# Performance work log

Measured on AMD Instinct MI355X. Metric: run time of the kernel, lower is better.

The kernel has to match this reference:

```python
import jax, jax.numpy as jnp
import numpy as np

D_MODEL = 1024
NUM_HEADS = 16
DEPTH = D_MODEL // NUM_HEADS


def setup_inputs() -> dict:
    key = jax.random.key(0)
    ks = jax.random.split(key, 11)
    B, S = 4, 2048
    scale = 1.0 / np.sqrt(D_MODEL)
    inp = {
        "query": jax.random.normal(ks[0], (B, S, D_MODEL), jnp.float32),
        "key": jax.random.normal(ks[1], (B, S, D_MODEL), jnp.float32),
        "value": jax.random.normal(ks[2], (B, S, D_MODEL), jnp.float32),
        # Linear params (torch nn.Linear: y = x @ W.T + b); store W as [out, in]
        "wq_w": jax.random.normal(ks[3], (D_MODEL, D_MODEL), jnp.float32) * scale,
        "wq_b": jnp.zeros((D_MODEL,), jnp.float32),
        "wk_w": jax.random.normal(ks[4], (D_MODEL, D_MODEL), jnp.float32) * scale,
        "wk_b": jnp.zeros((D_MODEL,), jnp.float32),
        "wv_w": jax.random.normal(ks[5], (D_MODEL, D_MODEL), jnp.float32) * scale,
        "wv_b": jnp.zeros((D_MODEL,), jnp.float32),
        "dense_w": jax.random.normal(ks[6], (D_MODEL, D_MODEL), jnp.float32) * scale,
        "dense_b": jnp.zeros((D_MODEL,), jnp.float32),
    }
    return inp


def _split_heads(x, B):
    # [B, S, D] -> [B, H, S, depth]
    return x.reshape(B, -1, NUM_HEADS, DEPTH).transpose(0, 2, 1, 3)


def reference(query, key, value, wq_w, wq_b, wk_w, wk_b, wv_w, wv_b, dense_w, dense_b):
    B = query.shape[0]
    q = _split_heads(query @ wq_w.T + wq_b, B)   # [B,H,Sq,depth]
    k = _split_heads(key @ wk_w.T + wk_b, B)     # [B,H,Sk,depth]
    v = _split_heads(value @ wv_w.T + wv_b, B)   # [B,H,Sk,depth]
    scores = jnp.einsum("bhqd,bhkd->bhqk", q, k) / jnp.sqrt(jnp.float32(DEPTH)).astype(q.dtype)
    attn = jax.nn.softmax(scores, axis=-1)
    out = jnp.einsum("bhqk,bhkd->bhqd", attn, v)  # [B,H,Sq,depth]
    out = out.transpose(0, 2, 1, 3).reshape(B, -1, D_MODEL)
    return out @ dense_w.T + dense_b
```

## Files before the change

kernel.cpp:

```cpp
#include <hip/hip_runtime.h>
#include <hip/hip_bf16.h>
#include <stdint.h>


#define SEQ    2048
#define DEPTH  64
#define HEADS  16
#define NMODEL 1024
#define MROWS  8192

typedef __bf16 bf16x8 __attribute__((ext_vector_type(8)));
typedef float  f32x4  __attribute__((ext_vector_type(4)));

__device__ __forceinline__ unsigned short f32_bf16(float f) {
    union { float f; unsigned int u; } c; c.f = f;
    unsigned int u = c.u + 0x7FFFu + ((c.u >> 16) & 1u);
    return (unsigned short)(u >> 16);
}

__device__ __forceinline__ void gload16(const unsigned short* g, unsigned short* l) {
    __builtin_amdgcn_global_load_lds(
        (const __attribute__((address_space(1))) unsigned int*)g,
        (__attribute__((address_space(3))) unsigned int*)l, 16, 0, 0);
}

__global__ __launch_bounds__(256) void cvt_flat_kernel(
    const float* __restrict__ a0, const float* __restrict__ a1, const float* __restrict__ a2,
    const float* __restrict__ w0, const float* __restrict__ w1,
    const float* __restrict__ w2, const float* __restrict__ w3,
    unsigned short* __restrict__ oa0, unsigned short* __restrict__ oa1,
    unsigned short* __restrict__ oa2,
    unsigned short* __restrict__ ow0, unsigned short* __restrict__ ow1,
    unsigned short* __restrict__ ow2, unsigned short* __restrict__ ow3)
{
    const unsigned int i = blockIdx.x * 256u + threadIdx.x;
    const unsigned int NA = 1u << 21;
    const unsigned int AW = 3u * NA;
    const float* in; unsigned short* out; unsigned int idx;
    if (i < AW) {
        const unsigned int p = i >> 21; idx = i & (NA - 1u);
        in  = (p == 0) ? a0 : (p == 1) ? a1 : a2;
        out = (p == 0) ? oa0 : (p == 1) ? oa1 : oa2;
    } else {
        const unsigned int j = i - AW;
        const unsigned int p = j >> 18; idx = j & ((1u << 18) - 1u);
        in  = (p == 0) ? w0 : (p == 1) ? w1 : (p == 2) ? w2 : w3;
        out = (p == 0) ? ow0 : (p == 1) ? ow1 : (p == 2) ? ow2 : ow3;
    }
    float4 f = ((const float4*)in)[idx];
    ushort4 o;
    o.x = f32_bf16(f.x); o.y = f32_bf16(f.y);
    o.z = f32_bf16(f.z); o.w = f32_bf16(f.w);
    ((ushort4*)out)[idx] = o;
}

__device__ __forceinline__ void gemm256_core(
    const unsigned short* __restrict__ A, const unsigned short* __restrict__ W,
    const float* __restrict__ bias, void* __restrict__ outp,
    int mode, float scale, int m0, int n0,
    unsigned short* __restrict__ Alds, unsigned short* __restrict__ Blds)
{
    const int tid  = threadIdx.x;
    const int wave = tid >> 6, lane = tid & 63;
    const int l15  = lane & 15, quad = lane >> 4;
    const int wr   = wave >> 1, wc = wave & 1;
    const int swz  = l15 & 7;
    const int K    = 1024;

    f32x4 acc[4][4] = {};

    const int trow = tid >> 3;
    const int tg   = ((tid & 7) ^ (trow & 7)) << 3;
    const unsigned short* Asrc[2][2];
    const unsigned short* Bsrc[2];
    #pragma unroll
    for (int u = 0; u < 2; ++u) {
        #pragma unroll
        for (int s = 0; s < 2; ++s)
            Asrc[u][s] = A + (size_t)(m0 + u * 128 + s * 64 + trow) * K + tg;
        Bsrc[u] = W + (size_t)(n0 + u * 64 + trow) * K + tg;
    }

    auto STAGE = [&](int buf, int kt2) {
        unsigned short* Ad = Alds + buf * 16384;
        unsigned short* Bd = Blds + buf * 8192;
        gload16(Asrc[0][0] + kt2 * 64, Ad + (      wave * 8) * 64);
        gload16(Asrc[0][1] + kt2 * 64, Ad + ( 64 + wave * 8) * 64);
        gload16(Asrc[1][0] + kt2 * 64, Ad + (128 + wave * 8) * 64);
        gload16(Asrc[1][1] + kt2 * 64, Ad + (192 + wave * 8) * 64);
        gload16(Bsrc[0]    + kt2 * 64, Bd + (      wave * 8) * 64);
        gload16(Bsrc[1]    + kt2 * 64, Bd + ( 64 + wave * 8) * 64);
    };

    STAGE(0, 0);
    STAGE(1, 1);
    asm volatile("s_waitcnt vmcnt(6)" ::: "memory");
    __builtin_amdgcn_s_barrier();

    const int arow = wr * 64 + l15;
    const int brow = wc * 64 + l15;

    for (int kt = 0; kt < 16; ++kt) {
        const unsigned short* Ab = Alds + (kt % 3) * 16384;
        const unsigned short* Bb = Blds + (kt % 3) * 8192;

        bf16x8 a0[4], b0[4];
        {
            const int pg = ((quad ^ swz) << 3);
            #pragma unroll
            for (int j = 0; j < 4; ++j)
                b0[j] = *(const bf16x8*)&Bb[(brow + j * 16) * 64 + pg];
            #pragma unroll
            for (int i = 0; i < 4; ++i)
                a0[i] = *(const bf16x8*)&Ab[(arow + i * 16) * 64 + pg];
        }
        if (kt + 2 < 16) STAGE((kt + 2) % 3, kt + 2);

        __builtin_amdgcn_s_setprio(1);
        #pragma unroll
        for (int i = 0; i < 4; ++i)
            #pragma unroll
            for (int j = 0; j < 4; ++j)
                acc[i][j] = __builtin_amdgcn_mfma_f32_16x16x32_bf16(a0[i], b0[j], acc[i][j], 0, 0, 0);
        __builtin_amdgcn_s_setprio(0);

        bf16x8 a1[4], b1[4];
        {
            const int pg = (((4 + quad) ^ swz) << 3);
            #pragma unroll
            for (int j = 0; j < 4; ++j)
                b1[j] = *(const bf16x8*)&Bb[(brow + j * 16) * 64 + pg];
            #pragma unroll
            for (int i = 0; i < 4; ++i)
                a1[i] = *(const bf16x8*)&Ab[(arow + i * 16) * 64 + pg];
        }
        __builtin_amdgcn_s_setprio(1);
        #pragma unroll
        for (int i = 0; i < 4; ++i)
            #pragma unroll
            for (int j = 0; j < 4; ++j)
                acc[i][j] = __builtin_amdgcn_mfma_f32_16x16x32_bf16(a1[i], b1[j], acc[i][j], 0, 0, 0);
        __builtin_amdgcn_s_setprio(0);

        if (kt + 2 < 16)
            asm volatile("s_waitcnt vmcnt(6)" ::: "memory");
        else
            asm volatile("s_waitcnt vmcnt(0)" ::: "memory");
        __builtin_amdgcn_s_barrier();
    }

    #pragma unroll
    for (int i = 0; i < 4; ++i) {
        #pragma unroll
        for (int j = 0; j < 4; ++j) {
            const int col = n0 + wc * 64 + j * 16 + l15;
            const int row_b = m0 + wr * 64 + i * 16 + quad * 4;
            if (mode == 2) {
                const int colp = (col & ~31)
                               | (col & 3)
                               | (((col >> 4) & 1) << 2)
                               | (((col >> 2) & 3) << 3);
                #pragma unroll
                for (int r = 0; r < 4; ++r) {
                    const int row = row_b + r;
                    ((unsigned short*)outp)[(size_t)row * MROWS + colp] =
                        f32_bf16(acc[i][j][r] + bias[row]);
                }
            } else if (mode == 0) {
                const float bv = bias[col];
                #pragma unroll
                for (int r = 0; r < 4; ++r)
                    ((float*)outp)[(size_t)(row_b + r) * NMODEL + col] = acc[i][j][r] + bv;
            } else {
                const float bv = bias[col];
                const int h_ = col >> 6, d_ = col & 63;
                #pragma unroll
                for (int r = 0; r < 4; ++r) {
                    const int row = row_b + r;
                    const int b_ = row >> 11, s_ = row & 2047;
                    ((unsigned short*)outp)[(((size_t)(b_ * HEADS + h_) * SEQ + s_) << 6) + d_] =
                        f32_bf16((acc[i][j][r] + bv) * scale);
                }
            }
        }
    }
}

__global__ __launch_bounds__(512, 2) void gemm_qkv(
    const unsigned short* __restrict__ qb,  const unsigned short* __restrict__ wqb,
    const float* __restrict__ bq, unsigned short* __restrict__ Qp,
    const unsigned short* __restrict__ kb,  const unsigned short* __restrict__ wkb,
    const float* __restrict__ bk, unsigned short* __restrict__ Kpj,
    const unsigned short* __restrict__ wvb, const unsigned short* __restrict__ vb,
    const float* __restrict__ bv, unsigned short* __restrict__ Vtg,
    float qscale)
{
    __shared__ unsigned short Alds[3 * 256 * 64];
    __shared__ unsigned short Blds[3 * 128 * 64];
    const int o = blockIdx.x, z = blockIdx.y;
    const int sid = (o & 7) * 32 + (o >> 3);
    if (z == 0) {
        gemm256_core(qb, wqb, bq, Qp, 1, qscale, (sid >> 3) * 256, (sid & 7) * 128, Alds, Blds);
    } else if (z == 1) {
        gemm256_core(kb, wkb, bk, Kpj, 1, 1.0f, (sid >> 3) * 256, (sid & 7) * 128, Alds, Blds);
    } else {
        gemm256_core(wvb, vb, bv, Vtg, 2, 1.0f, (sid & 3) * 256, (sid >> 2) * 128, Alds, Blds);
    }
}

__global__ __launch_bounds__(512, 2) void gemm_dense(
    const unsigned short* __restrict__ A, const unsigned short* __restrict__ W,
    const float* __restrict__ bias, float* __restrict__ out)
{
    __shared__ unsigned short Alds[3 * 256 * 64];
    __shared__ unsigned short Blds[3 * 128 * 64];
    const int o = blockIdx.x;
    const int sid = (o & 7) * 32 + (o >> 3);
    gemm256_core(A, W, bias, out, 0, 1.0f, (sid >> 3) * 256, (sid & 7) * 128, Alds, Blds);
}

__global__ __launch_bounds__(256, 2) void attn_fwd(
    const unsigned short* __restrict__ Qp,
    const unsigned short* __restrict__ Kp,
    const unsigned short* __restrict__ Vtg,
    unsigned short* __restrict__ Op)
{
    __shared__ unsigned short Klds[3 * 64 * 64];
    __shared__ unsigned short Vlds[3 * 64 * 64];
    const int tid  = threadIdx.x;
    const int wave = tid >> 6, lane = tid & 63;
    const int l15  = lane & 15, quad = lane >> 4;
    const int swz  = l15 & 7;
    const int bh   = blockIdx.y;
    const int b_   = bh >> 4, h_ = bh & 15;
    const int q0   = blockIdx.x * 256;

    const unsigned short* Qb = Qp + (size_t)bh * SEQ * DEPTH;
    const unsigned short* Kb = Kp + (size_t)bh * SEQ * DEPTH;
    const unsigned short* Vb = Vtg + (size_t)h_ * DEPTH * MROWS + (size_t)b_ * SEQ;

    const int srow = (wave << 3) + (lane >> 3);
    const int scg  = (lane & 7) ^ ((lane >> 3) & 7);

    const unsigned short* Kg0 = Kb + (size_t)srow * DEPTH + scg * 8;
    const unsigned short* Kg1 = Kb + (size_t)(srow + 32) * DEPTH + scg * 8;
    const unsigned short* Vg0 = Vb + (size_t)srow * MROWS + scg * 8;
    const unsigned short* Vg1 = Vb + (size_t)(srow + 32) * MROWS + scg * 8;

    bf16x8 qf[4][2];
    #pragma unroll
    for (int i = 0; i < 4; ++i)
        #pragma unroll
        for (int kc = 0; kc < 2; ++kc)
            qf[i][kc] = *(const bf16x8*)(Qb + (size_t)(q0 + wave * 64 + i * 16 + l15) * DEPTH
                                         + kc * 32 + quad * 8);

    union { bf16x8 v; unsigned short s[8]; } uo;
    #pragma unroll
    for (int j = 0; j < 8; ++j) uo.s[j] = 0x3F80;
    const bf16x8 ones = uo.v;

    f32x4 Ot[4][4] = {};
    f32x4 lacc[4]  = {};

    auto STAGE = [&](int buf, int kt) {
        unsigned short* KW = &Klds[buf * 4096 + wave * 512];
        unsigned short* VW = &Vlds[buf * 4096 + wave * 512];
        gload16(Kg0 + (size_t)kt * 4096, KW);
        gload16(Kg1 + (size_t)kt * 4096, KW + 2048);
        gload16(Vg0 + kt * 64, VW);
        gload16(Vg1 + kt * 64, VW + 2048);
    };

    STAGE(0, 0);
    STAGE(1, 1);
    asm volatile("s_waitcnt vmcnt(4)" ::: "memory");
    __builtin_amdgcn_s_barrier();

    const int NT = SEQ / 64;
    for (int kt = 0; kt < NT; ++kt) {
        const unsigned short* Kc = &Klds[(kt % 3) * 4096];
        const unsigned short* Vc = &Vlds[(kt % 3) * 4096];
        if (kt + 2 < NT) STAGE((kt + 2) % 3, kt + 2);

        f32x4 S[2][2][4];
        __builtin_amdgcn_s_setprio(1);
        #pragma unroll
        for (int half = 0; half < 2; ++half) {
            const int r0 = (2 * half) * 16 + l15;
            const int r1 = (2 * half + 1) * 16 + l15;
            bf16x8 ka0 = *(const bf16x8*)&Kc[r0 * 64 + ((quad ^ swz) << 3)];
            bf16x8 ka1 = *(const bf16x8*)&Kc[r0 * 64 + (((4 + quad) ^ swz) << 3)];
            bf16x8 kb0 = *(const bf16x8*)&Kc[r1 * 64 + ((quad ^ swz) << 3)];
            bf16x8 kb1 = *(const bf16x8*)&Kc[r1 * 64 + (((4 + quad) ^ swz) << 3)];
            #pragma unroll
            for (int i = 0; i < 4; ++i) {
                S[half][0][i] = f32x4{};
                S[half][0][i] = __builtin_amdgcn_mfma_f32_16x16x32_bf16(ka0, qf[i][0], S[half][0][i], 0, 0, 0);
                S[half][0][i] = __builtin_amdgcn_mfma_f32_16x16x32_bf16(ka1, qf[i][1], S[half][0][i], 0, 0, 0);
                S[half][1][i] = f32x4{};
                S[half][1][i] = __builtin_amdgcn_mfma_f32_16x16x32_bf16(kb0, qf[i][0], S[half][1][i], 0, 0, 0);
                S[half][1][i] = __builtin_amdgcn_mfma_f32_16x16x32_bf16(kb1, qf[i][1], S[half][1][i], 0, 0, 0);
            }
        }
        __builtin_amdgcn_s_setprio(0);

        bf16x8 pf0[4];
        #pragma unroll
        for (int i = 0; i < 4; ++i) {
            float e0 = __builtin_amdgcn_exp2f(S[0][0][i][0]);
            float e1 = __builtin_amdgcn_exp2f(S[0][0][i][1]);
            float e2 = __builtin_amdgcn_exp2f(S[0][0][i][2]);
            float e3 = __builtin_amdgcn_exp2f(S[0][0][i][3]);
            float e4 = __builtin_amdgcn_exp2f(S[0][1][i][0]);
            float e5 = __builtin_amdgcn_exp2f(S[0][1][i][1]);
            float e6 = __builtin_amdgcn_exp2f(S[0][1][i][2]);
            float e7 = __builtin_amdgcn_exp2f(S[0][1][i][3]);
            union { bf16x8 v; __hip_bfloat162 h[4]; } up;
            up.h[0] = __float22bfloat162_rn(make_float2(e0, e1));
            up.h[1] = __float22bfloat162_rn(make_float2(e2, e3));
            up.h[2] = __float22bfloat162_rn(make_float2(e4, e5));
            up.h[3] = __float22bfloat162_rn(make_float2(e6, e7));
            pf0[i] = up.v;
        }

        __builtin_amdgcn_s_setprio(1);
        lacc[0] = __builtin_amdgcn_mfma_f32_16x16x32_bf16(ones, pf0[0], lacc[0], 0, 0, 0);
        lacc[1] = __builtin_amdgcn_mfma_f32_16x16x32_bf16(ones, pf0[1], lacc[1], 0, 0, 0);
        lacc[2] = __builtin_amdgcn_mfma_f32_16x16x32_bf16(ones, pf0[2], lacc[2], 0, 0, 0);
        lacc[3] = __builtin_amdgcn_mfma_f32_16x16x32_bf16(ones, pf0[3], lacc[3], 0, 0, 0);
        #pragma unroll
        for (int dd = 0; dd < 4; ++dd) {
            bf16x8 vf = *(const bf16x8*)&Vc[(dd * 16 + l15) * 64 + ((quad ^ swz) << 3)];
            #pragma unroll
            for (int i = 0; i < 4; ++i)
                Ot[i][dd] = __builtin_amdgcn_mfma_f32_16x16x32_bf16(vf, pf0[i], Ot[i][dd], 0, 0, 0);
        }
        __builtin_amdgcn_s_setprio(0);

        bf16x8 pf1[4];
        #pragma unroll
        for (int i = 0; i < 4; ++i) {
            float e0 = __builtin_amdgcn_exp2f(S[1][0][i][0]);
            float e1 = __builtin_amdgcn_exp2f(S[1][0][i][1]);
            float e2 = __builtin_amdgcn_exp2f(S[1][0][i][2]);
            float e3 = __builtin_amdgcn_exp2f(S[1][0][i][3]);
            float e4 = __builtin_amdgcn_exp2f(S[1][1][i][0]);
            float e5 = __builtin_amdgcn_exp2f(S[1][1][i][1]);
            float e6 = __builtin_amdgcn_exp2f(S[1][1][i][2]);
            float e7 = __builtin_amdgcn_exp2f(S[1][1][i][3]);
            union { bf16x8 v; __hip_bfloat162 h[4]; } up;
            up.h[0] = __float22bfloat162_rn(make_float2(e0, e1));
            up.h[1] = __float22bfloat162_rn(make_float2(e2, e3));
            up.h[2] = __float22bfloat162_rn(make_float2(e4, e5));
            up.h[3] = __float22bfloat162_rn(make_float2(e6, e7));
            pf1[i] = up.v;
        }

        __builtin_amdgcn_s_setprio(1);
        lacc[0] = __builtin_amdgcn_mfma_f32_16x16x32_bf16(ones, pf1[0], lacc[0], 0, 0, 0);
        lacc[1] = __builtin_amdgcn_mfma_f32_16x16x32_bf16(ones, pf1[1], lacc[1], 0, 0, 0);
        lacc[2] = __builtin_amdgcn_mfma_f32_16x16x32_bf16(ones, pf1[2], lacc[2], 0, 0, 0);
        lacc[3] = __builtin_amdgcn_mfma_f32_16x16x32_bf16(ones, pf1[3], lacc[3], 0, 0, 0);
        #pragma unroll
        for (int dd = 0; dd < 4; ++dd) {
            bf16x8 vf = *(const bf16x8*)&Vc[(dd * 16 + l15) * 64 + (((4 + quad) ^ swz) << 3)];
            #pragma unroll
            for (int i = 0; i < 4; ++i)
                Ot[i][dd] = __builtin_amdgcn_mfma_f32_16x16x32_bf16(vf, pf1[i], Ot[i][dd], 0, 0, 0);
        }
        __builtin_amdgcn_s_setprio(0);

        if (kt + 2 < NT)
            asm volatile("s_waitcnt vmcnt(4)" ::: "memory");
        else
            asm volatile("s_waitcnt vmcnt(0)" ::: "memory");
        __builtin_amdgcn_s_barrier();
    }

    #pragma unroll
    for (int i = 0; i < 4; ++i) {
        const float inv = 1.0f / lacc[i][0];
        const int row = b_ * SEQ + q0 + wave * 64 + i * 16 + l15;
        #pragma unroll
        for (int dd = 0; dd < 4; ++dd) {
            ushort4 ov;
            ov.x = f32_bf16(Ot[i][dd][0] * inv);
            ov.y = f32_bf16(Ot[i][dd][1] * inv);
            ov.z = f32_bf16(Ot[i][dd][2] * inv);
            ov.w = f32_bf16(Ot[i][dd][3] * inv);
            const int col = h_ * 64 + dd * 16 + quad * 4;
            *(ushort4*)&Op[(size_t)row * NMODEL + col] = ov;
        }
    }
}

extern "C" void kernel_launch(void* const* d_in, const int* in_sizes, int n_in,
                              void* d_out, int out_size, void* d_ws, size_t ws_size,
                              hipStream_t stream) {
    const float* q  = (const float*)d_in[0];
    const float* k  = (const float*)d_in[1];
    const float* v  = (const float*)d_in[2];
    const float* wq = (const float*)d_in[3];
    const float* bq = (const float*)d_in[4];
    const float* wk = (const float*)d_in[5];
    const float* bk = (const float*)d_in[6];
    const float* wv = (const float*)d_in[7];
    const float* bv = (const float*)d_in[8];
    const float* wd = (const float*)d_in[9];
    const float* bd = (const float*)d_in[10];

    char* ws = (char*)d_ws;
    size_t off = 0;
    auto alloc = [&](size_t bytes) { char* p = ws + off; off += bytes; return p; };
    const size_t ACT = (size_t)MROWS * NMODEL * 2;
    const size_t WGT = (size_t)NMODEL * NMODEL * 2;

    unsigned short* qb   = (unsigned short*)alloc(ACT);
    unsigned short* kb   = (unsigned short*)alloc(ACT);
    unsigned short* vb   = (unsigned short*)alloc(ACT);
    unsigned short* wqb  = (unsigned short*)alloc(WGT);
    unsigned short* wkb  = (unsigned short*)alloc(WGT);
    unsigned short* wvb  = (unsigned short*)alloc(WGT);
    unsigned short* wdb  = (unsigned short*)alloc(WGT);
    unsigned short* Qp   = (unsigned short*)alloc(ACT);
    unsigned short* Kpj  = (unsigned short*)alloc(ACT);
    unsigned short* Vtg  = (unsigned short*)alloc(ACT);
    unsigned short* attn = (unsigned short*)alloc(ACT);

    cvt_flat_kernel<<<28672, 256, 0, stream>>>(
        q, k, v, wq, wk, wv, wd, qb, kb, vb, wqb, wkb, wvb, wdb);

    const float SC = 0.18033688011112042f;
    gemm_qkv<<<dim3(256, 3), 512, 0, stream>>>(qb, wqb, bq, Qp,
                                               kb, wkb, bk, Kpj,
                                               wvb, vb, bv, Vtg, SC);

    attn_fwd<<<dim3(SEQ / 256, 64), 256, 0, stream>>>(Qp, Kpj, Vtg, attn);

    gemm_dense<<<256, 512, 0, stream>>>(attn, wdb, bd, (float*)d_out);
}
```

Baseline: 319.0 us.

## Enlarge GEMM tiles to 256x256 with eight-phase ping-pong LDS pipeline

```diff
diff --git a/kernel.cpp b/kernel.cpp
--- a/kernel.cpp
+++ b/kernel.cpp
@@ -11,6 +11,8 @@
 
 typedef __bf16 bf16x8 __attribute__((ext_vector_type(8)));
 typedef float  f32x4  __attribute__((ext_vector_type(4)));
+
+#define MFMA16 __builtin_amdgcn_mfma_f32_16x16x32_bf16
 
 __device__ __forceinline__ unsigned short f32_bf16(float f) {
     union { float f; unsigned int u; } c; c.f = f;
@@ -58,103 +60,93 @@
     const unsigned short* __restrict__ A, const unsigned short* __restrict__ W,
     const float* __restrict__ bias, void* __restrict__ outp,
     int mode, float scale, int m0, int n0,
-    unsigned short* __restrict__ Alds, unsigned short* __restrict__ Blds)
+    unsigned short* __restrict__ Abuf, unsigned short* __restrict__ Bbuf)
 {
     const int tid  = threadIdx.x;
     const int wave = tid >> 6, lane = tid & 63;
     const int l15  = lane & 15, quad = lane >> 4;
-    const int wr   = wave >> 1, wc = wave & 1;
+    const int wr   = wave >> 2, wc = wave & 3;
     const int swz  = l15 & 7;
     const int K    = 1024;
 
-    f32x4 acc[4][4] = {};
+    f32x4 acc[8][4] = {};
 
     const int trow = tid >> 3;
     const int tg   = ((tid & 7) ^ (trow & 7)) << 3;
-    const unsigned short* Asrc[2][2];
-    const unsigned short* Bsrc[2];
+    const int dstw = wave * 512;
+
+    const unsigned short* Asw[4];
+    const unsigned short* Bsw[4];
     #pragma unroll
-    for (int u = 0; u < 2; ++u) {
-        #pragma unroll
-        for (int s = 0; s < 2; ++s)
-            Asrc[u][s] = A + (size_t)(m0 + u * 128 + s * 64 + trow) * K + tg;
-        Bsrc[u] = W + (size_t)(n0 + u * 64 + trow) * K + tg;
-    }
-
-    auto STAGE = [&](int buf, int kt2) {
-        unsigned short* Ad = Alds + buf * 16384;
-        unsigned short* Bd = Blds + buf * 8192;
-        gload16(Asrc[0][0] + kt2 * 64, Ad + (      wave * 8) * 64);
-        gload16(Asrc[0][1] + kt2 * 64, Ad + ( 64 + wave * 8) * 64);
-        gload16(Asrc[1][0] + kt2 * 64, Ad + (128 + wave * 8) * 64);
-        gload16(Asrc[1][1] + kt2 * 64, Ad + (192 + wave * 8) * 64);
-        gload16(Bsrc[0]    + kt2 * 64, Bd + (      wave * 8) * 64);
-        gload16(Bsrc[1]    + kt2 * 64, Bd + ( 64 + wave * 8) * 64);
-    };
-
-    STAGE(0, 0);
-    STAGE(1, 1);
-    asm volatile("s_waitcnt vmcnt(6)" ::: "memory");
+    for (int sw = 0; sw < 4; ++sw) {
+        Asw[sw] = A + (size_t)(m0 + sw * 64 + trow) * K + tg;
+        const int rp  = sw * 64 + trow;
+        const int nh  = rp >> 7, wcb = (rp >> 5) & 3, rem = rp & 31;
+        Bsw[sw] = W + (size_t)(n0 + wcb * 64 + nh * 32 + rem) * K + tg;
+    }
+
+#define SA_(c, sw, kt) gload16(Asw[sw] + (kt) * 64, Abuf + (c) * 16384 + (sw) * 4096 + dstw)
+#define SB_(c, sw, kt) gload16(Bsw[sw] + (kt) * 64, Bbuf + (c) * 16384 + (sw) * 4096 + dstw)
+
+    SA_(0, 0, 0); SA_(0, 1, 0); SA_(0, 2, 0); SA_(0, 3, 0);
+    SB_(0, 0, 0); SB_(0, 1, 0); SB_(0, 2, 0); SB_(0, 3, 0);
+    SB_(1, 0, 1); SB_(1, 1, 1); SA_(1, 0, 1); SA_(1, 2, 1);
+    asm volatile("s_waitcnt vmcnt(4)" ::: "memory");
     __builtin_amdgcn_s_barrier();
 
-    const int arow = wr * 64 + l15;
-    const int brow = wc * 64 + l15;
-
-    for (int kt = 0; kt < 16; ++kt) {
-        const unsigned short* Ab = Alds + (kt % 3) * 16384;
-        const unsigned short* Bb = Blds + (kt % 3) * 8192;
-
-        bf16x8 a0[4], b0[4];
-        {
-            const int pg = ((quad ^ swz) << 3);
-            #pragma unroll
-            for (int j = 0; j < 4; ++j)
-                b0[j] = *(const bf16x8*)&Bb[(brow + j * 16) * 64 + pg];
-            #pragma unroll
-            for (int i = 0; i < 4; ++i)
-                a0[i] = *(const bf16x8*)&Ab[(arow + i * 16) * 64 + pg];
-        }
-        if (kt + 2 < 16) STAGE((kt + 2) % 3, kt + 2);
-
-        __builtin_amdgcn_s_setprio(1);
-        #pragma unroll
-        for (int i = 0; i < 4; ++i)
-            #pragma unroll
-            for (int j = 0; j < 4; ++j)
-                acc[i][j] = __builtin_amdgcn_mfma_f32_16x16x32_bf16(a0[i], b0[j], acc[i][j], 0, 0, 0);
-        __builtin_amdgcn_s_setprio(0);
-
-        bf16x8 a1[4], b1[4];
-        {
-            const int pg = (((4 + quad) ^ swz) << 3);
-            #pragma unroll
-            for (int j = 0; j < 4; ++j)
-                b1[j] = *(const bf16x8*)&Bb[(brow + j * 16) * 64 + pg];
-            #pragma unroll
-            for (int i = 0; i < 4; ++i)
-                a1[i] = *(const bf16x8*)&Ab[(arow + i * 16) * 64 + pg];
-        }
-        __builtin_amdgcn_s_setprio(1);
-        #pragma unroll
-        for (int i = 0; i < 4; ++i)
-            #pragma unroll
-            for (int j = 0; j < 4; ++j)
-                acc[i][j] = __builtin_amdgcn_mfma_f32_16x16x32_bf16(a1[i], b1[j], acc[i][j], 0, 0, 0);
-        __builtin_amdgcn_s_setprio(0);
-
-        if (kt + 2 < 16)
-            asm volatile("s_waitcnt vmcnt(6)" ::: "memory");
-        else
-            asm volatile("s_waitcnt vmcnt(0)" ::: "memory");
-        __builtin_amdgcn_s_barrier();
-    }
+#define PHASE_(c, mh, nh, STG, DOVM) do {                                        \
+    const unsigned short* Ab_ = Abuf + (c) * 16384;                              \
+    const unsigned short* Bb_ = Bbuf + (c) * 16384;                              \
+    bf16x8 a_[4][2], b_[2][2];                                                   \
+    _Pragma("unroll")                                                            \
+    for (int i4 = 0; i4 < 4; ++i4) {                                             \
+        const int row = wr * 128 + ((mh) * 4 + i4) * 16 + l15;                   \
+        a_[i4][0] = *(const bf16x8*)&Ab_[row * 64 + ((quad ^ swz) << 3)];        \
+        a_[i4][1] = *(const bf16x8*)&Ab_[row * 64 + (((4 + quad) ^ swz) << 3)];  \
+    }                                                                            \
+    _Pragma("unroll")                                                            \
+    for (int j2 = 0; j2 < 2; ++j2) {                                             \
+        const int row = (nh) * 128 + wc * 32 + j2 * 16 + l15;                    \
+        b_[j2][0] = *(const bf16x8*)&Bb_[row * 64 + ((quad ^ swz) << 3)];        \
+        b_[j2][1] = *(const bf16x8*)&Bb_[row * 64 + (((4 + quad) ^ swz) << 3)];  \
+    }                                                                            \
+    STG;                                                                         \
+    __builtin_amdgcn_s_barrier();                                                \
+    __builtin_amdgcn_s_setprio(1);                                               \
+    _Pragma("unroll")                                                            \
+    for (int i4 = 0; i4 < 4; ++i4)                                               \
+        _Pragma("unroll")                                                        \
+        for (int j2 = 0; j2 < 2; ++j2) {                                         \
+            acc[(mh)*4+i4][(nh)*2+j2] = MFMA16(a_[i4][0], b_[j2][0], acc[(mh)*4+i4][(nh)*2+j2], 0, 0, 0); \
+            acc[(mh)*4+i4][(nh)*2+j2] = MFMA16(a_[i4][1], b_[j2][1], acc[(mh)*4+i4][(nh)*2+j2], 0, 0, 0); \
+        }                                                                        \
+    __builtin_amdgcn_s_setprio(0);                                               \
+    if (DOVM) asm volatile("s_waitcnt vmcnt(4)" ::: "memory");                   \
+    __builtin_amdgcn_s_barrier();                                                \
+} while (0)
+
+    for (int it = 0; it < 8; ++it) {
+        const int t1 = 2 * it + 1, t2 = 2 * it + 2, t3 = 2 * it + 3;
+        const bool h2 = t2 < 16, h3 = t3 < 16;
+        PHASE_(0, 0, 0, { SA_(1, 1, t1); SA_(1, 3, t1); }, false);
+        PHASE_(0, 1, 0, { SB_(1, 2, t1); SB_(1, 3, t1); }, false);
+        PHASE_(0, 0, 1, { if (h2) { SB_(0, 0, t2); SB_(0, 1, t2); } }, false);
+        PHASE_(0, 1, 1, { if (h2) { SA_(0, 0, t2); SA_(0, 2, t2); } }, true);
+        PHASE_(1, 0, 0, { if (h2) { SA_(0, 1, t2); SA_(0, 3, t2); } }, false);
+        PHASE_(1, 1, 0, { if (h2) { SB_(0, 2, t2); SB_(0, 3, t2); } }, false);
+        PHASE_(1, 0, 1, { if (h3) { SB_(1, 0, t3); SB_(1, 1, t3); } }, false);
+        PHASE_(1, 1, 1, { if (h3) { SA_(1, 0, t3); SA_(1, 2, t3); } }, it + 1 < 8);
+    }
+#undef PHASE_
+#undef SA_
+#undef SB_
 
     #pragma unroll
-    for (int i = 0; i < 4; ++i) {
+    for (int i = 0; i < 8; ++i) {
         #pragma unroll
         for (int j = 0; j < 4; ++j) {
             const int col = n0 + wc * 64 + j * 16 + l15;
-            const int row_b = m0 + wr * 64 + i * 16 + quad * 4;
+            const int row_b = m0 + wr * 128 + i * 16 + quad * 4;
             if (mode == 2) {
                 const int colp = (col & ~31)
                                | (col & 3)
@@ -195,16 +187,16 @@
     const float* __restrict__ bv, unsigned short* __restrict__ Vtg,
     float qscale)
 {
-    __shared__ unsigned short Alds[3 * 256 * 64];
-    __shared__ unsigned short Blds[3 * 128 * 64];
+    __shared__ unsigned short Abuf[2 * 16384];
+    __shared__ unsigned short Bbuf[2 * 16384];
     const int o = blockIdx.x, z = blockIdx.y;
-    const int sid = (o & 7) * 32 + (o >> 3);
+    const int sid = (o & 7) * 16 + (o >> 3);
     if (z == 0) {
-        gemm256_core(qb, wqb, bq, Qp, 1, qscale, (sid >> 3) * 256, (sid & 7) * 128, Alds, Blds);
+        gemm256_core(qb, wqb, bq, Qp, 1, qscale, (sid >> 2) * 256, (sid & 3) * 256, Abuf, Bbuf);
     } else if (z == 1) {
-        gemm256_core(kb, wkb, bk, Kpj, 1, 1.0f, (sid >> 3) * 256, (sid & 7) * 128, Alds, Blds);
+        gemm256_core(kb, wkb, bk, Kpj, 1, 1.0f, (sid >> 2) * 256, (sid & 3) * 256, Abuf, Bbuf);
     } else {
-        gemm256_core(wvb, vb, bv, Vtg, 2, 1.0f, (sid & 3) * 256, (sid >> 2) * 128, Alds, Blds);
+        gemm256_core(wvb, vb, bv, Vtg, 2, 1.0f, (sid & 3) * 256, (sid >> 2) * 256, Abuf, Bbuf);
     }
 }
 
@@ -212,11 +204,11 @@
     const unsigned short* __restrict__ A, const unsigned short* __restrict__ W,
     const float* __restrict__ bias, float* __restrict__ out)
 {
-    __shared__ unsigned short Alds[3 * 256 * 64];
-    __shared__ unsigned short Blds[3 * 128 * 64];
+    __shared__ unsigned short Abuf[2 * 16384];
+    __shared__ unsigned short Bbuf[2 * 16384];
     const int o = blockIdx.x;
-    const int sid = (o & 7) * 32 + (o >> 3);
-    gemm256_core(A, W, bias, out, 0, 1.0f, (sid >> 3) * 256, (sid & 7) * 128, Alds, Blds);
+    const int sid = (o & 7) * 16 + (o >> 3);
+    gemm256_core(A, W, bias, out, 0, 1.0f, (sid >> 2) * 256, (sid & 3) * 256, Abuf, Bbuf);
 }
 
 __global__ __launch_bounds__(256, 2) void attn_fwd(
@@ -296,11 +288,11 @@
             #pragma unroll
             for (int i = 0; i < 4; ++i) {
                 S[half][0][i] = f32x4{};
-                S[half][0][i] = __builtin_amdgcn_mfma_f32_16x16x32_bf16(ka0, qf[i][0], S[half][0][i], 0, 0, 0);
-                S[half][0][i] = __builtin_amdgcn_mfma_f32_16x16x32_bf16(ka1, qf[i][1], S[half][0][i], 0, 0, 0);
+                S[half][0][i] = MFMA16(ka0, qf[i][0], S[half][0][i], 0, 0, 0);
+                S[half][0][i] = MFMA16(ka1, qf[i][1], S[half][0][i], 0, 0, 0);
                 S[half][1][i] = f32x4{};
-                S[half][1][i] = __builtin_amdgcn_mfma_f32_16x16x32_bf16(kb0, qf[i][0], S[half][1][i], 0, 0, 0);
-                S[half][1][i] = __builtin_amdgcn_mfma_f32_16x16x32_bf16(kb1, qf[i][1], S[half][1][i], 0, 0, 0);
+                S[half][1][i] = MFMA16(kb0, qf[i][0], S[half][1][i], 0, 0, 0);
+                S[half][1][i] = MFMA16(kb1, qf[i][1], S[half][1][i], 0, 0, 0);
             }
         }
         __builtin_amdgcn_s_setprio(0);
@@ -325,16 +317,16 @@
         }
 
         __builtin_amdgcn_s_setprio(1);
-        lacc[0] = __builtin_amdgcn_mfma_f32_16x16x32_bf16(ones, pf0[0], lacc[0], 0, 0, 0);
-        lacc[1] = __builtin_amdgcn_mfma_f32_16x16x32_bf16(ones, pf0[1], lacc[1], 0, 0, 0);
-        lacc[2] = __builtin_amdgcn_mfma_f32_16x16x32_bf16(ones, pf0[2], lacc[2], 0, 0, 0);
-        lacc[3] = __builtin_amdgcn_mfma_f32_16x16x32_bf16(ones, pf0[3], lacc[3], 0, 0, 0);
+        lacc[0] = MFMA16(ones, pf0[0], lacc[0], 0, 0, 0);
+        lacc[1] = MFMA16(ones, pf0[1], lacc[1], 0, 0, 0);
+        lacc[2] = MFMA16(ones, pf0[2], lacc[2], 0, 0, 0);
+        lacc[3] = MFMA16(ones, pf0[3], lacc[3], 0, 0, 0);
         #pragma unroll
         for (int dd = 0; dd < 4; ++dd) {
             bf16x8 vf = *(const bf16x8*)&Vc[(dd * 16 + l15) * 64 + ((quad ^ swz) << 3)];
             #pragma unroll
             for (int i = 0; i < 4; ++i)
-                Ot[i][dd] = __builtin_amdgcn_mfma_f32_16x16x32_bf16(vf, pf0[i], Ot[i][dd], 0, 0, 0);
+                Ot[i][dd] = MFMA16(vf, pf0[i], Ot[i][dd], 0, 0, 0);
         }
         __builtin_amdgcn_s_setprio(0);
 
@@ -358,16 +350,16 @@
         }
 
         __builtin_amdgcn_s_setprio(1);
-        lacc[0] = __builtin_amdgcn_mfma_f32_16x16x32_bf16(ones, pf1[0], lacc[0], 0, 0, 0);
-        lacc[1] = __builtin_amdgcn_mfma_f32_16x16x32_bf16(ones, pf1[1], lacc[1], 0, 0, 0);
-        lacc[2] = __builtin_amdgcn_mfma_f32_16x16x32_bf16(ones, pf1[2], lacc[2], 0, 0, 0);
-        lacc[3] = __builtin_amdgcn_mfma_f32_16x16x32_bf16(ones, pf1[3], lacc[3], 0, 0, 0);
+        lacc[0] = MFMA16(ones, pf1[0], lacc[0], 0, 0, 0);
+        lacc[1] = MFMA16(ones, pf1[1], lacc[1], 0, 0, 0);
+        lacc[2] = MFMA16(ones, pf1[2], lacc[2], 0, 0, 0);
+        lacc[3] = MFMA16(ones, pf1[3], lacc[3], 0, 0, 0);
         #pragma unroll
         for (int dd = 0; dd < 4; ++dd) {
             bf16x8 vf = *(const bf16x8*)&Vc[(dd * 16 + l15) * 64 + (((4 + quad) ^ swz) << 3)];
             #pragma unroll
             for (int i = 0; i < 4; ++i)
-                Ot[i][dd] = __builtin_amdgcn_mfma_f32_16x16x32_bf16(vf, pf1[i], Ot[i][dd], 0, 0, 0);
+                Ot[i][dd] = MFMA16(vf, pf1[i], Ot[i][dd], 0, 0, 0);
         }
         __builtin_amdgcn_s_setprio(0);
 
@@ -432,11 +424,11 @@
         q, k, v, wq, wk, wv, wd, qb, kb, vb, wqb, wkb, wvb, wdb);
 
     const float SC = 0.18033688011112042f;
-    gemm_qkv<<<dim3(256, 3), 512, 0, stream>>>(qb, wqb, bq, Qp,
+    gemm_qkv<<<dim3(128, 3), 512, 0, stream>>>(qb, wqb, bq, Qp,
                                                kb, wkb, bk, Kpj,
                                                wvb, vb, bv, Vtg, SC);
 
     attn_fwd<<<dim3(SEQ / 256, 64), 256, 0, stream>>>(Qp, Kpj, Vtg, attn);
 
-    gemm_dense<<<256, 512, 0, stream>>>(attn, wdb, bd, (float*)d_out);
-}
+    gemm_dense<<<128, 512, 0, stream>>>(attn, wdb, bd, (float*)d_out);
+}
```

Measured after the change: 335.2 us. +5.1%, slower.

## Split attention query tile across 8 waves with double-buffered K/V staging

Applied to the files above, without the earlier changes.

```diff
diff --git a/kernel.cpp b/kernel.cpp
--- a/kernel.cpp
+++ b/kernel.cpp
@@ -11,6 +11,8 @@
 
 typedef __bf16 bf16x8 __attribute__((ext_vector_type(8)));
 typedef float  f32x4  __attribute__((ext_vector_type(4)));
+
+#define MFMA16 __builtin_amdgcn_mfma_f32_16x16x32_bf16
 
 __device__ __forceinline__ unsigned short f32_bf16(float f) {
     union { float f; unsigned int u; } c; c.f = f;
@@ -121,7 +123,7 @@
         for (int i = 0; i < 4; ++i)
             #pragma unroll
             for (int j = 0; j < 4; ++j)
-                acc[i][j] = __builtin_amdgcn_mfma_f32_16x16x32_bf16(a0[i], b0[j], acc[i][j], 0, 0, 0);
+                acc[i][j] = MFMA16(a0[i], b0[j], acc[i][j], 0, 0, 0);
         __builtin_amdgcn_s_setprio(0);
 
         bf16x8 a1[4], b1[4];
@@ -139,7 +141,7 @@
         for (int i = 0; i < 4; ++i)
             #pragma unroll
             for (int j = 0; j < 4; ++j)
-                acc[i][j] = __builtin_amdgcn_mfma_f32_16x16x32_bf16(a1[i], b1[j], acc[i][j], 0, 0, 0);
+                acc[i][j] = MFMA16(a1[i], b1[j], acc[i][j], 0, 0, 0);
         __builtin_amdgcn_s_setprio(0);
 
         if (kt + 2 < 16)
@@ -219,14 +221,14 @@
     gemm256_core(A, W, bias, out, 0, 1.0f, (sid >> 3) * 256, (sid & 7) * 128, Alds, Blds);
 }
 
-__global__ __launch_bounds__(256, 2) void attn_fwd(
+__global__ __launch_bounds__(512, 2) void attn_fwd(
     const unsigned short* __restrict__ Qp,
     const unsigned short* __restrict__ Kp,
     const unsigned short* __restrict__ Vtg,
     unsigned short* __restrict__ Op)
 {
-    __shared__ unsigned short Klds[3 * 64 * 64];
-    __shared__ unsigned short Vlds[3 * 64 * 64];
+    __shared__ unsigned short Klds[2 * 64 * 64];
+    __shared__ unsigned short Vlds[2 * 64 * 64];
     const int tid  = threadIdx.x;
     const int wave = tid >> 6, lane = tid & 63;
     const int l15  = lane & 15, quad = lane >> 4;
@@ -239,20 +241,18 @@
     const unsigned short* Kb = Kp + (size_t)bh * SEQ * DEPTH;
     const unsigned short* Vb = Vtg + (size_t)h_ * DEPTH * MROWS + (size_t)b_ * SEQ;
 
-    const int srow = (wave << 3) + (lane >> 3);
-    const int scg  = (lane & 7) ^ ((lane >> 3) & 7);
-
-    const unsigned short* Kg0 = Kb + (size_t)srow * DEPTH + scg * 8;
-    const unsigned short* Kg1 = Kb + (size_t)(srow + 32) * DEPTH + scg * 8;
-    const unsigned short* Vg0 = Vb + (size_t)srow * MROWS + scg * 8;
-    const unsigned short* Vg1 = Vb + (size_t)(srow + 32) * MROWS + scg * 8;
-
-    bf16x8 qf[4][2];
+    const int srow = tid >> 3;
+    const int scg  = (tid & 7) ^ (srow & 7);
+    const unsigned short* Kgp = Kb + (size_t)srow * DEPTH + scg * 8;
+    const unsigned short* Vgp = Vb + (size_t)srow * MROWS + scg * 8;
+    const int dstw = wave * 512;
+
+    bf16x8 qf[2][2];
     #pragma unroll
-    for (int i = 0; i < 4; ++i)
+    for (int i = 0; i < 2; ++i)
         #pragma unroll
         for (int kc = 0; kc < 2; ++kc)
-            qf[i][kc] = *(const bf16x8*)(Qb + (size_t)(q0 + wave * 64 + i * 16 + l15) * DEPTH
+            qf[i][kc] = *(const bf16x8*)(Qb + (size_t)(q0 + wave * 32 + i * 16 + l15) * DEPTH
                                          + kc * 32 + quad * 8);
 
     union { bf16x8 v; unsigned short s[8]; } uo;
@@ -260,30 +260,27 @@
     for (int j = 0; j < 8; ++j) uo.s[j] = 0x3F80;
     const bf16x8 ones = uo.v;
 
-    f32x4 Ot[4][4] = {};
-    f32x4 lacc[4]  = {};
+    f32x4 Ot[2][4] = {};
+    f32x4 lacc[2]  = {};
 
     auto STAGE = [&](int buf, int kt) {
-        unsigned short* KW = &Klds[buf * 4096 + wave * 512];
-        unsigned short* VW = &Vlds[buf * 4096 + wave * 512];
-        gload16(Kg0 + (size_t)kt * 4096, KW);
-        gload16(Kg1 + (size_t)kt * 4096, KW + 2048);
-        gload16(Vg0 + kt * 64, VW);
-        gload16(Vg1 + kt * 64, VW + 2048);
+        gload16(Kgp + (size_t)kt * 4096, &Klds[buf * 4096 + dstw]);
+        gload16(Vgp + kt * 64,           &Vlds[buf * 4096 + dstw]);
     };
 
     STAGE(0, 0);
-    STAGE(1, 1);
-    asm volatile("s_waitcnt vmcnt(4)" ::: "memory");
+    asm volatile("s_waitcnt vmcnt(0)" ::: "memory");
     __builtin_amdgcn_s_barrier();
 
     const int NT = SEQ / 64;
     for (int kt = 0; kt < NT; ++kt) {
-        const unsigned short* Kc = &Klds[(kt % 3) * 4096];
-        const unsigned short* Vc = &Vlds[(kt % 3) * 4096];
-        if (kt + 2 < NT) STAGE((kt + 2) % 3, kt + 2);
-
-        f32x4 S[2][2][4];
+        const int cur = kt & 1;
+        if (kt + 1 < NT) STAGE(cur ^ 1, kt + 1);
+
+        const unsigned short* Kc = &Klds[cur * 4096];
+        const unsigned short* Vc = &Vlds[cur * 4096];
+
+        f32x4 S[2][2][2];
         __builtin_amdgcn_s_setprio(1);
         #pragma unroll
         for (int half = 0; half < 2; ++half) {
@@ -294,20 +291,20 @@
             bf16x8 kb0 = *(const bf16x8*)&Kc[r1 * 64 + ((quad ^ swz) << 3)];
             bf16x8 kb1 = *(const bf16x8*)&Kc[r1 * 64 + (((4 + quad) ^ swz) << 3)];
             #pragma unroll
-            for (int i = 0; i < 4; ++i) {
+            for (int i = 0; i < 2; ++i) {
                 S[half][0][i] = f32x4{};
-                S[half][0][i] = __builtin_amdgcn_mfma_f32_16x16x32_bf16(ka0, qf[i][0], S[half][0][i], 0, 0, 0);
-                S[half][0][i] = __builtin_amdgcn_mfma_f32_16x16x32_bf16(ka1, qf[i][1], S[half][0][i], 0, 0, 0);
+                S[half][0][i] = MFMA16(ka0, qf[i][0], S[half][0][i], 0, 0, 0);
+                S[half][0][i] = MFMA16(ka1, qf[i][1], S[half][0][i], 0, 0, 0);
                 S[half][1][i] = f32x4{};
-                S[half][1][i] = __builtin_amdgcn_mfma_f32_16x16x32_bf16(kb0, qf[i][0], S[half][1][i], 0, 0, 0);
-                S[half][1][i] = __builtin_amdgcn_mfma_f32_16x16x32_bf16(kb1, qf[i][1], S[half][1][i], 0, 0, 0);
+                S[half][1][i] = MFMA16(kb0, qf[i][0], S[half][1][i], 0, 0, 0);
+                S[half][1][i] = MFMA16(kb1, qf[i][1], S[half][1][i], 0, 0, 0);
             }
         }
         __builtin_amdgcn_s_setprio(0);
 
-        bf16x8 pf0[4];
-        #pragma unroll
-        for (int i = 0; i < 4; ++i) {
+        bf16x8 pf0[2];
+        #pragma unroll
+        for (int i = 0; i < 2; ++i) {
             float e0 = __builtin_amdgcn_exp2f(S[0][0][i][0]);
             float e1 = __builtin_amdgcn_exp2f(S[0][0][i][1]);
             float e2 = __builtin_amdgcn_exp2f(S[0][0][i][2]);
@@ -325,22 +322,19 @@
         }
 
         __builtin_amdgcn_s_setprio(1);
-        lacc[0] = __builtin_amdgcn_mfma_f32_16x16x32_bf16(ones, pf0[0], lacc[0], 0, 0, 0);
-        lacc[1] = __builtin_amdgcn_mfma_f32_16x16x32_bf16(ones, pf0[1], lacc[1], 0, 0, 0);
-        lacc[2] = __builtin_amdgcn_mfma_f32_16x16x32_bf16(ones, pf0[2], lacc[2], 0, 0, 0);
-        lacc[3] = __builtin_amdgcn_mfma_f32_16x16x32_bf16(ones, pf0[3], lacc[3], 0, 0, 0);
+        lacc[0] = MFMA16(ones, pf0[0], lacc[0], 0, 0, 0);
+        lacc[1] = MFMA16(ones, pf0[1], lacc[1], 0, 0, 0);
         #pragma unroll
         for (int dd = 0; dd < 4; ++dd) {
             bf16x8 vf = *(const bf16x8*)&Vc[(dd * 16 + l15) * 64 + ((quad ^ swz) << 3)];
-            #pragma unroll
-            for (int i = 0; i < 4; ++i)
-                Ot[i][dd] = __builtin_amdgcn_mfma_f32_16x16x32_bf16(vf, pf0[i], Ot[i][dd], 0, 0, 0);
+            Ot[0][dd] = MFMA16(vf, pf0[0], Ot[0][dd], 0, 0, 0);
+            Ot[1][dd] = MFMA16(vf, pf0[1], Ot[1][dd], 0, 0, 0);
         }
         __builtin_amdgcn_s_setprio(0);
 
-        bf16x8 pf1[4];
-        #pragma unroll
-        for (int i = 0; i < 4; ++i) {
+        bf16x8 pf1[2];
+        #pragma unroll
+        for (int i = 0; i < 2; ++i) {
             float e0 = __builtin_amdgcn_exp2f(S[1][0][i][0]);
             float e1 = __builtin_amdgcn_exp2f(S[1][0][i][1]);
             float e2 = __builtin_amdgcn_exp2f(S[1][0][i][2]);
@@ -358,30 +352,24 @@
         }
 
         __builtin_amdgcn_s_setprio(1);
-        lacc[0] = __builtin_amdgcn_mfma_f32_16x16x32_bf16(ones, pf1[0], lacc[0], 0, 0, 0);
-        lacc[1] = __builtin_amdgcn_mfma_f32_16x16x32_bf16(ones, pf1[1], lacc[1], 0, 0, 0);
-        lacc[2] = __builtin_amdgcn_mfma_f32_16x16x32_bf16(ones, pf1[2], lacc[2], 0, 0, 0);
-        lacc[3] = __builtin_amdgcn_mfma_f32_16x16x32_bf16(ones, pf1[3], lacc[3], 0, 0, 0);
+        lacc[0] = MFMA16(ones, pf1[0], lacc[0], 0, 0, 0);
+        lacc[1] = MFMA16(ones, pf1[1], lacc[1], 0, 0, 0);
         #pragma unroll
         for (int dd = 0; dd < 4; ++dd) {
             bf16x8 vf = *(const bf16x8*)&Vc[(dd * 16 + l15) * 64 + (((4 + quad) ^ swz) << 3)];
-            #pragma unroll
-            for (int i = 0; i < 4; ++i)
-                Ot[i][dd] = __builtin_amdgcn_mfma_f32_16x16x32_bf16(vf, pf1[i], Ot[i][dd], 0, 0, 0);
+            Ot[0][dd] = MFMA16(vf, pf1[0], Ot[0][dd], 0, 0, 0);
+            Ot[1][dd] = MFMA16(vf, pf1[1], Ot[1][dd], 0, 0, 0);
         }
         __builtin_amdgcn_s_setprio(0);
 
-        if (kt + 2 < NT)
-            asm volatile("s_waitcnt vmcnt(4)" ::: "memory");
-        else
-            asm volatile("s_waitcnt vmcnt(0)" ::: "memory");
+        asm volatile("s_waitcnt vmcnt(0)" ::: "memory");
         __builtin_amdgcn_s_barrier();
     }
 
     #pragma unroll
-    for (int i = 0; i < 4; ++i) {
+    for (int i = 0; i < 2; ++i) {
         const float inv = 1.0f / lacc[i][0];
-        const int row = b_ * SEQ + q0 + wave * 64 + i * 16 + l15;
+        const int row = b_ * SEQ + q0 + wave * 32 + i * 16 + l15;
         #pragma unroll
         for (int dd = 0; dd < 4; ++dd) {
             ushort4 ov;
@@ -436,7 +424,7 @@
                                                kb, wkb, bk, Kpj,
                                                wvb, vb, bv, Vtg, SC);
 
-    attn_fwd<<<dim3(SEQ / 256, 64), 256, 0, stream>>>(Qp, Kpj, Vtg, attn);
+    attn_fwd<<<dim3(SEQ / 256, 64), 512, 0, stream>>>(Qp, Kpj, Vtg, attn);
 
     gemm_dense<<<256, 512, 0, stream>>>(attn, wdb, bd, (float*)d_out);
 }
```

After: 315.4 us. About the same (-1.1%).
